# Performance work log

Measured on AMD Instinct MI355X. Metric: run time of the kernel, lower is better.

## Reference

```python
import jax, jax.numpy as jnp
import numpy as np

N_NODES = 50000
N_EDGES = 800000
IN_FEATS = 96
HIDDEN = 48


def setup_inputs() -> dict:
    key = jax.random.key(0)
    ks = jax.random.split(key, 16)
    x = jax.random.normal(ks[0], (N_NODES, IN_FEATS), dtype=jnp.float32)
    edge_index = jax.random.randint(ks[1], (2, N_EDGES), 0, N_NODES, dtype=jnp.int32)

    def lin(k, fan_in, fan_out):
        s = 1.0 / np.sqrt(fan_in)
        return jax.random.uniform(k, (fan_in, fan_out), jnp.float32, -s, s)

    return {
        "x": x,
        "edge_index": edge_index,
        # SAGEConv layer 0: in -> hidden
        "w_self0": lin(ks[2], IN_FEATS, HIDDEN),
        "w_neigh0": lin(ks[3], IN_FEATS, HIDDEN),
        "b0": jnp.zeros((HIDDEN,), jnp.float32),
        # SAGEConv layer 1: hidden -> hidden
        "w_self1": lin(ks[4], HIDDEN, HIDDEN),
        "w_neigh1": lin(ks[5], HIDDEN, HIDDEN),
        "b1": jnp.zeros((HIDDEN,), jnp.float32),
        # SAGEConv layer 2: hidden -> hidden
        "w_self2": lin(ks[6], HIDDEN, HIDDEN),
        "w_neigh2": lin(ks[7], HIDDEN, HIDDEN),
        "b2": jnp.zeros((HIDDEN,), jnp.float32),
        # prediction head: hidden -> 1
        "w_pred": lin(ks[8], HIDDEN, 1),
        "b_pred": jnp.zeros((1,), jnp.float32),
    }


def _sage_mean(x, src, dst, deg_inv, w_self, w_neigh, b):
    # mean over in-neighbors: gather src features, segment-sum at dst, / in-degree
    agg = jax.ops.segment_sum(x[src], dst, num_segments=N_NODES) * deg_inv  # [N, F]
    return x @ w_self + agg @ w_neigh + b


def reference(x, edge_index, w_self0, w_neigh0, b0, w_self1, w_neigh1, b1,
              w_self2, w_neigh2, b2, w_pred, b_pred):
    src, dst = edge_index[0], edge_index[1]
    deg = jax.ops.segment_sum(jnp.ones((src.shape[0],), x.dtype), dst,
                              num_segments=N_NODES)
    deg_inv = (1.0 / jnp.maximum(deg, 1.0))[:, None]  # isolated nodes -> 0 agg

    h = jax.nn.relu(_sage_mean(x, src, dst, deg_inv, w_self0, w_neigh0, b0))
    h = jax.nn.relu(_sage_mean(h, src, dst, deg_inv, w_self1, w_neigh1, b1))
    h = jax.nn.relu(_sage_mean(h, src, dst, deg_inv, w_self2, w_neigh2, b2))
    return h @ w_pred + b_pred  # [N, 1]
```

## Files before the change

### kernel.cpp

```cpp
#include <hip/hip_runtime.h>
#include <hip/hip_fp16.h>


constexpr int HID = 48;
constexpr int MAXDEG = 64;
constexpr int GNB = 64;

__device__ __forceinline__ unsigned pack_h2(float a, float b) {
    __half2 h = __floats2half2_rn(a, b);
    return *reinterpret_cast<unsigned*>(&h);
}
__device__ __forceinline__ void acc_u2(float* g, uint2 u) {
    __half2 h0 = *reinterpret_cast<__half2*>(&u.x);
    __half2 h1 = *reinterpret_cast<__half2*>(&u.y);
    float2 f0 = __half22float2(h0), f1 = __half22float2(h1);
    g[0] += f0.x; g[1] += f0.y; g[2] += f1.x; g[3] += f1.y;
}
__device__ __forceinline__ void unpack_u2(float* v, uint2 u) {
    __half2 h0 = *reinterpret_cast<__half2*>(&u.x);
    __half2 h1 = *reinterpret_cast<__half2*>(&u.y);
    float2 f0 = __half22float2(h0), f1 = __half22float2(h1);
    v[0] = f0.x; v[1] = f0.y; v[2] = f1.x; v[3] = f1.y;
}
__device__ __forceinline__ void fma12_h(const uint2* __restrict__ wrow, float s,
                                        float* acc) {
    uint2 w0 = wrow[0], w1 = wrow[1], w2 = wrow[2];
    float v[12];
    unpack_u2(v + 0, w0); unpack_u2(v + 4, w1); unpack_u2(v + 8, w2);
#pragma unroll
    for (int j = 0; j < 12; ++j) acc[j] = fmaf(s, v[j], acc[j]);
}

__device__ __forceinline__ void gather_h4(const __half* __restrict__ p,
                                          const unsigned short* __restrict__ bkt,
                                          int deg, int e, int jb, float* g) {
    float ga[12], gb[12];
#pragma unroll
    for (int j = 0; j < 12; ++j) { ga[j] = 0.0f; gb[j] = 0.0f; }
    int i = e;
    for (; i + 6 < deg; i += 8) {
        int s0 = bkt[i], s1 = bkt[i + 2], s2 = bkt[i + 4], s3 = bkt[i + 6];
        const uint2* r0 = reinterpret_cast<const uint2*>(p + (size_t)s0 * HID + jb);
        const uint2* r1 = reinterpret_cast<const uint2*>(p + (size_t)s1 * HID + jb);
        const uint2* r2 = reinterpret_cast<const uint2*>(p + (size_t)s2 * HID + jb);
        const uint2* r3 = reinterpret_cast<const uint2*>(p + (size_t)s3 * HID + jb);
        uint2 a0 = r0[0], a1 = r0[1], a2 = r0[2];
        uint2 b0 = r1[0], b1 = r1[1], b2 = r1[2];
        uint2 c0 = r2[0], c1 = r2[1], c2 = r2[2];
        uint2 d0 = r3[0], d1 = r3[1], d2 = r3[2];
        acc_u2(ga + 0, a0); acc_u2(ga + 4, a1); acc_u2(ga + 8, a2);
        acc_u2(gb + 0, b0); acc_u2(gb + 4, b1); acc_u2(gb + 8, b2);
        acc_u2(ga + 0, c0); acc_u2(ga + 4, c1); acc_u2(ga + 8, c2);
        acc_u2(gb + 0, d0); acc_u2(gb + 4, d1); acc_u2(gb + 8, d2);
    }
    for (; i + 2 < deg; i += 4) {
        int s0 = bkt[i], s1 = bkt[i + 2];
        const uint2* r0 = reinterpret_cast<const uint2*>(p + (size_t)s0 * HID + jb);
        const uint2* r1 = reinterpret_cast<const uint2*>(p + (size_t)s1 * HID + jb);
        uint2 a0 = r0[0], a1 = r0[1], a2 = r0[2];
        uint2 b0 = r1[0], b1 = r1[1], b2 = r1[2];
        acc_u2(ga + 0, a0); acc_u2(ga + 4, a1); acc_u2(ga + 8, a2);
        acc_u2(gb + 0, b0); acc_u2(gb + 4, b1); acc_u2(gb + 8, b2);
    }
    if (i < deg) {
        const uint2* r0 = reinterpret_cast<const uint2*>(p + (size_t)bkt[i] * HID + jb);
        uint2 a0 = r0[0], a1 = r0[1], a2 = r0[2];
        acc_u2(ga + 0, a0); acc_u2(ga + 4, a1); acc_u2(ga + 8, a2);
    }
#pragma unroll
    for (int j = 0; j < 12; ++j) g[j] = ga[j] + gb[j];
#pragma unroll
    for (int j = 0; j < 12; ++j) g[j] += __shfl_xor(g[j], 4, 64);
}

__global__ __launch_bounds__(128) void fill_proj_k(
    const float* __restrict__ X, const float* __restrict__ Wn,
    const float* __restrict__ Ws, const float* __restrict__ bias,
    __half* __restrict__ p_out, float* __restrict__ s_out, int n_nodes,
    const int* __restrict__ src, const int* __restrict__ dst,
    int* __restrict__ cnt, unsigned short* __restrict__ buckets,
    int n_edges, int gemm_blocks) {
    __shared__ float wlds[96 * HID];
    __shared__ float bias_lds[HID];
    const int t = threadIdx.x;

    if ((int)blockIdx.x >= gemm_blocks) {
        int base = (blockIdx.x - gemm_blocks) * 256 + t;
        int e0 = base, e1 = base + 128;
        if (e0 < n_edges) {
            int d = dst[e0];
            int s = src[e0];
            int pos = atomicAdd(&cnt[d], 1);
            if (pos < MAXDEG) buckets[(size_t)d * MAXDEG + pos] = (unsigned short)s;
        }
        if (e1 < n_edges) {
            int d = dst[e1];
            int s = src[e1];
            int pos = atomicAdd(&cnt[d], 1);
            if (pos < MAXDEG) buckets[(size_t)d * MAXDEG + pos] = (unsigned short)s;
        }
        return;
    }

    const int q = t & 3;
    const int m = t >> 2;
    const int jb = q * 12;
    const int n0 = blockIdx.x * GNB + 2 * m;
    const int n1 = n0 + 1;
    const bool v0 = n0 < n_nodes, v1 = n1 < n_nodes;
    const int cn0 = v0 ? n0 : 0, cn1 = v1 ? n1 : 0;
    const float4* xr0 = reinterpret_cast<const float4*>(X + (size_t)cn0 * 96);
    const float4* xr1 = reinterpret_cast<const float4*>(X + (size_t)cn1 * 96);

    for (int i = t; i < 96 * HID; i += 128) wlds[i] = Wn[i];
    __syncthreads();
    {
        float pa[12], pb[12];
#pragma unroll
        for (int j = 0; j < 12; ++j) { pa[j] = 0.0f; pb[j] = 0.0f; }
#pragma unroll 4
        for (int k4 = 0; k4 < 24; ++k4) {
            float4 xa = xr0[k4];
            float4 xb = xr1[k4];
#pragma unroll
            for (int c = 0; c < 4; ++c) {
                float x0 = (c == 0) ? xa.x : (c == 1) ? xa.y : (c == 2) ? xa.z : xa.w;
                float x1 = (c == 0) ? xb.x : (c == 1) ? xb.y : (c == 2) ? xb.z : xb.w;
                const float4* wr =
                    reinterpret_cast<const float4*>(&wlds[(k4 * 4 + c) * HID + jb]);
#pragma unroll
                for (int j4 = 0; j4 < 3; ++j4) {
                    float4 wv = wr[j4];
                    pa[j4 * 4 + 0] = fmaf(x0, wv.x, pa[j4 * 4 + 0]);
                    pa[j4 * 4 + 1] = fmaf(x0, wv.y, pa[j4 * 4 + 1]);
                    pa[j4 * 4 + 2] = fmaf(x0, wv.z, pa[j4 * 4 + 2]);
                    pa[j4 * 4 + 3] = fmaf(x0, wv.w, pa[j4 * 4 + 3]);
                    pb[j4 * 4 + 0] = fmaf(x1, wv.x, pb[j4 * 4 + 0]);
                    pb[j4 * 4 + 1] = fmaf(x1, wv.y, pb[j4 * 4 + 1]);
                    pb[j4 * 4 + 2] = fmaf(x1, wv.z, pb[j4 * 4 + 2]);
                    pb[j4 * 4 + 3] = fmaf(x1, wv.w, pb[j4 * 4 + 3]);
                }
            }
        }
        if (v0) {
            uint2* po = reinterpret_cast<uint2*>(p_out + (size_t)n0 * HID + jb);
            po[0] = make_uint2(pack_h2(pa[0], pa[1]), pack_h2(pa[2], pa[3]));
            po[1] = make_uint2(pack_h2(pa[4], pa[5]), pack_h2(pa[6], pa[7]));
            po[2] = make_uint2(pack_h2(pa[8], pa[9]), pack_h2(pa[10], pa[11]));
        }
        if (v1) {
            uint2* po = reinterpret_cast<uint2*>(p_out + (size_t)n1 * HID + jb);
            po[0] = make_uint2(pack_h2(pb[0], pb[1]), pack_h2(pb[2], pb[3]));
            po[1] = make_uint2(pack_h2(pb[4], pb[5]), pack_h2(pb[6], pb[7]));
            po[2] = make_uint2(pack_h2(pb[8], pb[9]), pack_h2(pb[10], pb[11]));
        }
    }
    __syncthreads();

    for (int i = t; i < 96 * HID; i += 128) wlds[i] = Ws[i];
    if (t < HID) bias_lds[t] = bias[t];
    __syncthreads();
    {
        float sa[12], sb[12];
#pragma unroll
        for (int j = 0; j < 12; ++j) {
            float b = bias_lds[jb + j];
            sa[j] = b; sb[j] = b;
        }
#pragma unroll 4
        for (int k4 = 0; k4 < 24; ++k4) {
            float4 xa = xr0[k4];
            float4 xb = xr1[k4];
#pragma unroll
            for (int c = 0; c < 4; ++c) {
                float x0 = (c == 0) ? xa.x : (c == 1) ? xa.y : (c == 2) ? xa.z : xa.w;
                float x1 = (c == 0) ? xb.x : (c == 1) ? xb.y : (c == 2) ? xb.z : xb.w;
                const float4* wr =
                    reinterpret_cast<const float4*>(&wlds[(k4 * 4 + c) * HID + jb]);
#pragma unroll
                for (int j4 = 0; j4 < 3; ++j4) {
                    float4 wv = wr[j4];
                    sa[j4 * 4 + 0] = fmaf(x0, wv.x, sa[j4 * 4 + 0]);
                    sa[j4 * 4 + 1] = fmaf(x0, wv.y, sa[j4 * 4 + 1]);
                    sa[j4 * 4 + 2] = fmaf(x0, wv.z, sa[j4 * 4 + 2]);
                    sa[j4 * 4 + 3] = fmaf(x0, wv.w, sa[j4 * 4 + 3]);
                    sb[j4 * 4 + 0] = fmaf(x1, wv.x, sb[j4 * 4 + 0]);
                    sb[j4 * 4 + 1] = fmaf(x1, wv.y, sb[j4 * 4 + 1]);
                    sb[j4 * 4 + 2] = fmaf(x1, wv.z, sb[j4 * 4 + 2]);
                    sb[j4 * 4 + 3] = fmaf(x1, wv.w, sb[j4 * 4 + 3]);
                }
            }
        }
        float4* so0 = reinterpret_cast<float4*>(s_out + (size_t)cn0 * HID + jb);
        float4* so1 = reinterpret_cast<float4*>(s_out + (size_t)cn1 * HID + jb);
#pragma unroll
        for (int j4 = 0; j4 < 3; ++j4) {
            if (v0) so0[j4] = make_float4(sa[j4 * 4 + 0], sa[j4 * 4 + 1],
                                          sa[j4 * 4 + 2], sa[j4 * 4 + 3]);
            if (v1) so1[j4] = make_float4(sb[j4 * 4 + 0], sb[j4 * 4 + 1],
                                          sb[j4 * 4 + 2], sb[j4 * 4 + 3]);
        }
    }
}

__global__ __launch_bounds__(128, 6) void act_k(
    const __half* __restrict__ p_in, const float* __restrict__ s_in,
    const int* __restrict__ cnt, const unsigned short* __restrict__ buckets,
    __half* __restrict__ h_out, int n_nodes) {
    const int t = threadIdx.x;
    const int q = t & 3;
    const int e = (t >> 2) & 1;
    const int m = t >> 3;
    const int n = blockIdx.x * 16 + m;
    if (n >= n_nodes) return;
    const int jb = q * 12;

    const int deg = min(cnt[n], MAXDEG);
    const float di = 1.0f / fmaxf((float)deg, 1.0f);
    float g[12];
    gather_h4(p_in, buckets + (size_t)n * MAXDEG, deg, e, jb, g);

    if (e == 0) {
        const float4* sr = reinterpret_cast<const float4*>(s_in + (size_t)n * HID + jb);
        float h[12];
#pragma unroll
        for (int j4 = 0; j4 < 3; ++j4) {
            float4 sv = sr[j4];
            h[j4 * 4 + 0] = fmaxf(fmaf(di, g[j4 * 4 + 0], sv.x), 0.0f);
            h[j4 * 4 + 1] = fmaxf(fmaf(di, g[j4 * 4 + 1], sv.y), 0.0f);
            h[j4 * 4 + 2] = fmaxf(fmaf(di, g[j4 * 4 + 2], sv.z), 0.0f);
            h[j4 * 4 + 3] = fmaxf(fmaf(di, g[j4 * 4 + 3], sv.w), 0.0f);
        }
        uint2* ho = reinterpret_cast<uint2*>(h_out + (size_t)n * HID + jb);
        ho[0] = make_uint2(pack_h2(h[0], h[1]), pack_h2(h[2], h[3]));
        ho[1] = make_uint2(pack_h2(h[4], h[5]), pack_h2(h[6], h[7]));
        ho[2] = make_uint2(pack_h2(h[8], h[9]), pack_h2(h[10], h[11]));
    }
}

template <bool LAST>
__global__ __launch_bounds__(128, 6) void layer_k(
    const __half* __restrict__ h_in, const int* __restrict__ cnt,
    const unsigned short* __restrict__ buckets, const float* __restrict__ wn,
    const float* __restrict__ ws, const float* __restrict__ bn,
    const float* __restrict__ w_pred, const float* __restrict__ b_pred,
    __half* __restrict__ h_out, float* __restrict__ out, int n_nodes) {
    __shared__ uint2 wn_s[HID * HID / 4];
    __shared__ uint2 ws_s[HID * HID / 4];
    __shared__ float bn_lds[HID];
    __shared__ float wp_lds[HID];

    const int t = threadIdx.x;
    for (int i4 = t; i4 < HID * HID / 4; i4 += 128) {
        float4 a = reinterpret_cast<const float4*>(wn)[i4];
        float4 b = reinterpret_cast<const float4*>(ws)[i4];
        wn_s[i4] = make_uint2(pack_h2(a.x, a.y), pack_h2(a.z, a.w));
        ws_s[i4] = make_uint2(pack_h2(b.x, b.y), pack_h2(b.z, b.w));
    }
    if (t < HID) bn_lds[t] = bn[t];
    if (LAST && t < HID) wp_lds[t] = w_pred[t];
    __syncthreads();

    const int q = t & 3;
    const int e = (t >> 2) & 1;
    const int m = t >> 3;
    const int n = blockIdx.x * 16 + m;
    if (n >= n_nodes) return;
    const int jb = q * 12;

    const int deg = min(cnt[n], MAXDEG);
    const float di = 1.0f / fmaxf((float)deg, 1.0f);
    float g[12];
    gather_h4(h_in, buckets + (size_t)n * MAXDEG, deg, e, jb, g);
#pragma unroll
    for (int j = 0; j < 12; ++j) g[j] *= di;

    float hs_own[12];
    {
        const uint2* hr = reinterpret_cast<const uint2*>(h_in + (size_t)n * HID + jb);
        uint2 a = hr[0], b = hr[1], c = hr[2];
        unpack_u2(hs_own + 0, a); unpack_u2(hs_own + 4, b); unpack_u2(hs_own + 8, c);
    }

    float acc[12];
#pragma unroll
    for (int j = 0; j < 12; ++j) acc[j] = (e == 0) ? bn_lds[jb + j] : 0.0f;

    const int kb = e * 24;
#pragma unroll
    for (int kk = 0; kk < 24; ++kk) {
        const int k = kb + kk;
        const int srcl = (t & ~3) | (k / 12);
        float gs = __shfl(g[kk % 12], srcl, 64);
        float hv = __shfl(hs_own[kk % 12], srcl, 64);
        fma12_h(&wn_s[(k * HID + jb) >> 2], gs, acc);
        fma12_h(&ws_s[(k * HID + jb) >> 2], hv, acc);
    }
#pragma unroll
    for (int j = 0; j < 12; ++j) acc[j] += __shfl_xor(acc[j], 4, 64);

    if (LAST) {
        float s = 0.0f;
#pragma unroll
        for (int j = 0; j < 12; ++j) s = fmaf(fmaxf(acc[j], 0.0f), wp_lds[jb + j], s);
        s += __shfl_xor(s, 1, 64);
        s += __shfl_xor(s, 2, 64);
        if ((t & 7) == 0) out[n] = s + b_pred[0];
        return;
    }

    if (e == 0) {
        float h[12];
#pragma unroll
        for (int j = 0; j < 12; ++j) h[j] = fmaxf(acc[j], 0.0f);
        uint2* ho = reinterpret_cast<uint2*>(h_out + (size_t)n * HID + jb);
        ho[0] = make_uint2(pack_h2(h[0], h[1]), pack_h2(h[2], h[3]));
        ho[1] = make_uint2(pack_h2(h[4], h[5]), pack_h2(h[6], h[7]));
        ho[2] = make_uint2(pack_h2(h[8], h[9]), pack_h2(h[10], h[11]));
    }
}

extern "C" void kernel_launch(void* const* d_in, const int* in_sizes, int n_in,
                              void* d_out, int out_size, void* d_ws, size_t ws_size,
                              hipStream_t stream) {
    const float* x        = (const float*)d_in[0];
    const int*   ei       = (const int*)d_in[1];
    const float* w_self0  = (const float*)d_in[2];
    const float* w_neigh0 = (const float*)d_in[3];
    const float* b0       = (const float*)d_in[4];
    const float* w_self1  = (const float*)d_in[5];
    const float* w_neigh1 = (const float*)d_in[6];
    const float* b1       = (const float*)d_in[7];
    const float* w_self2  = (const float*)d_in[8];
    const float* w_neigh2 = (const float*)d_in[9];
    const float* b2       = (const float*)d_in[10];
    const float* w_pred   = (const float*)d_in[11];
    const float* b_pred   = (const float*)d_in[12];

    const int n_nodes = in_sizes[0] / 96;
    const int n_edges = in_sizes[1] / 2;
    const int* src = ei;
    const int* dst = ei + n_edges;

    char* wsb = (char*)d_ws;
    int* cnt                = (int*)wsb;              wsb += (size_t)n_nodes * 4;
    unsigned short* buckets = (unsigned short*)wsb;   wsb += (size_t)n_nodes * MAXDEG * 2;
    __half* p0 = (__half*)wsb;                        wsb += (size_t)n_nodes * HID * 2;
    __half* h1 = (__half*)wsb;                        wsb += (size_t)n_nodes * HID * 2;
    __half* h2 = (__half*)wsb;                        wsb += (size_t)n_nodes * HID * 2;
    float* s0 = (float*)wsb;                          wsb += (size_t)n_nodes * HID * 4;
    float* out = (float*)d_out;

    const int gnb = (n_nodes + GNB - 1) / GNB;
    const int fb = (n_edges + 255) / 256;
    const int lb = (n_nodes + 15) / 16;

    hipMemsetAsync(cnt, 0, (size_t)n_nodes * 4, stream);

    fill_proj_k<<<gnb + fb, 128, 0, stream>>>(x, w_neigh0, w_self0, b0, p0, s0,
                                              n_nodes, src, dst, cnt, buckets,
                                              n_edges, gnb);
    act_k<<<lb, 128, 0, stream>>>(p0, s0, cnt, buckets, h1, n_nodes);
    layer_k<false><<<lb, 128, 0, stream>>>(h1, cnt, buckets, w_neigh1, w_self1,
                                           b1, nullptr, nullptr, h2, nullptr,
                                           n_nodes);
    layer_k<true><<<lb, 128, 0, stream>>>(h2, cnt, buckets, w_neigh2, w_self2,
                                          b2, w_pred, b_pred, nullptr, out,
                                          n_nodes);
}
```

Measured before the change: 208.7 us.

## Prefetch bucket indices and unroll first 16 neighbor gathers with zero-row padding

Loads the first 16 neighbor indices as two vector loads and gathers them unconditionally, substituting a zeroed padding row for slots beyond the degree, so more independent loads are in flight. Layer kernels issue the count, bucket and self-feature loads before the shared-memory weight fill so they overlap. Degree counters are spaced by a stride of 4 to reduce atomic contention, and the edge-fill blocks process 4 edges per thread. Low-degree nodes now issue extra loads of the padding row, and the workspace grows slightly.

```diff
diff --git a/kernel.cpp b/kernel.cpp
--- a/kernel.cpp
+++ b/kernel.cpp
@@ -31,13 +31,52 @@
     for (int j = 0; j < 12; ++j) acc[j] = fmaf(s, v[j], acc[j]);
 }
 
-__device__ __forceinline__ void gather_h4(const __half* __restrict__ p,
+__device__ __forceinline__ void gather_h8(const __half* __restrict__ p,
                                           const unsigned short* __restrict__ bkt,
-                                          int deg, int e, int jb, float* g) {
+                                          uint4 pv0, uint4 pv1, int deg, int e,
+                                          int jb, int zrow, float* g) {
     float ga[12], gb[12];
 #pragma unroll
     for (int j = 0; j < 12; ++j) { ga[j] = 0.0f; gb[j] = 0.0f; }
-    int i = e;
+    const int sh = 16 * e;
+    int idx[8];
+    {
+        unsigned w[8] = {pv0.x, pv0.y, pv0.z, pv0.w, pv1.x, pv1.y, pv1.z, pv1.w};
+#pragma unroll
+        for (int r = 0; r < 8; ++r) {
+            int k = 2 * r + e;
+            idx[r] = (k < deg) ? (int)((w[r] >> sh) & 0xffffu) : zrow;
+        }
+    }
+    {
+        const uint2* r0 = reinterpret_cast<const uint2*>(p + (size_t)idx[0] * HID + jb);
+        const uint2* r1 = reinterpret_cast<const uint2*>(p + (size_t)idx[1] * HID + jb);
+        const uint2* r2 = reinterpret_cast<const uint2*>(p + (size_t)idx[2] * HID + jb);
+        const uint2* r3 = reinterpret_cast<const uint2*>(p + (size_t)idx[3] * HID + jb);
+        uint2 a0 = r0[0], a1 = r0[1], a2 = r0[2];
+        uint2 b0 = r1[0], b1 = r1[1], b2 = r1[2];
+        uint2 c0 = r2[0], c1 = r2[1], c2 = r2[2];
+        uint2 d0 = r3[0], d1 = r3[1], d2 = r3[2];
+        acc_u2(ga + 0, a0); acc_u2(ga + 4, a1); acc_u2(ga + 8, a2);
+        acc_u2(gb + 0, b0); acc_u2(gb + 4, b1); acc_u2(gb + 8, b2);
+        acc_u2(ga + 0, c0); acc_u2(ga + 4, c1); acc_u2(ga + 8, c2);
+        acc_u2(gb + 0, d0); acc_u2(gb + 4, d1); acc_u2(gb + 8, d2);
+    }
+    {
+        const uint2* r0 = reinterpret_cast<const uint2*>(p + (size_t)idx[4] * HID + jb);
+        const uint2* r1 = reinterpret_cast<const uint2*>(p + (size_t)idx[5] * HID + jb);
+        const uint2* r2 = reinterpret_cast<const uint2*>(p + (size_t)idx[6] * HID + jb);
+        const uint2* r3 = reinterpret_cast<const uint2*>(p + (size_t)idx[7] * HID + jb);
+        uint2 a0 = r0[0], a1 = r0[1], a2 = r0[2];
+        uint2 b0 = r1[0], b1 = r1[1], b2 = r1[2];
+        uint2 c0 = r2[0], c1 = r2[1], c2 = r2[2];
+        uint2 d0 = r3[0], d1 = r3[1], d2 = r3[2];
+        acc_u2(ga + 0, a0); acc_u2(ga + 4, a1); acc_u2(ga + 8, a2);
+        acc_u2(gb + 0, b0); acc_u2(gb + 4, b1); acc_u2(gb + 8, b2);
+        acc_u2(ga + 0, c0); acc_u2(ga + 4, c1); acc_u2(ga + 8, c2);
+        acc_u2(gb + 0, d0); acc_u2(gb + 4, d1); acc_u2(gb + 8, d2);
+    }
+    int i = 16 + e;
     for (; i + 6 < deg; i += 8) {
         int s0 = bkt[i], s1 = bkt[i + 2], s2 = bkt[i + 4], s3 = bkt[i + 6];
         const uint2* r0 = reinterpret_cast<const uint2*>(p + (size_t)s0 * HID + jb);
@@ -79,28 +118,28 @@
     __half* __restrict__ p_out, float* __restrict__ s_out, int n_nodes,
     const int* __restrict__ src, const int* __restrict__ dst,
     int* __restrict__ cnt, unsigned short* __restrict__ buckets,
-    int n_edges, int gemm_blocks) {
+    int n_edges, int gemm_blocks, int cstride) {
     __shared__ float wlds[96 * HID];
     __shared__ float bias_lds[HID];
     const int t = threadIdx.x;
 
     if ((int)blockIdx.x >= gemm_blocks) {
-        int base = (blockIdx.x - gemm_blocks) * 256 + t;
-        int e0 = base, e1 = base + 128;
-        if (e0 < n_edges) {
-            int d = dst[e0];
-            int s = src[e0];
-            int pos = atomicAdd(&cnt[d], 1);
-            if (pos < MAXDEG) buckets[(size_t)d * MAXDEG + pos] = (unsigned short)s;
-        }
-        if (e1 < n_edges) {
-            int d = dst[e1];
-            int s = src[e1];
-            int pos = atomicAdd(&cnt[d], 1);
-            if (pos < MAXDEG) buckets[(size_t)d * MAXDEG + pos] = (unsigned short)s;
+        int base = (blockIdx.x - gemm_blocks) * 512 + t;
+#pragma unroll
+        for (int u = 0; u < 4; ++u) {
+            int eidx = base + u * 128;
+            if (eidx < n_edges) {
+                int d = dst[eidx];
+                int s = src[eidx];
+                int pos = atomicAdd(&cnt[(size_t)d * cstride], 1);
+                if (pos < MAXDEG) buckets[(size_t)d * MAXDEG + pos] = (unsigned short)s;
+            }
         }
         return;
     }
+
+    if (blockIdx.x == 0 && t < 24)
+        reinterpret_cast<unsigned*>(p_out + (size_t)n_nodes * HID)[t] = 0u;
 
     const int q = t & 3;
     const int m = t >> 2;
@@ -206,8 +245,10 @@
 __global__ __launch_bounds__(128, 6) void act_k(
     const __half* __restrict__ p_in, const float* __restrict__ s_in,
     const int* __restrict__ cnt, const unsigned short* __restrict__ buckets,
-    __half* __restrict__ h_out, int n_nodes) {
+    __half* __restrict__ h_out, int n_nodes, int cstride) {
     const int t = threadIdx.x;
+    if (blockIdx.x == 0 && t < 24)
+        reinterpret_cast<unsigned*>(h_out + (size_t)n_nodes * HID)[t] = 0u;
     const int q = t & 3;
     const int e = (t >> 2) & 1;
     const int m = t >> 3;
@@ -215,22 +256,35 @@
     if (n >= n_nodes) return;
     const int jb = q * 12;
 
-    const int deg = min(cnt[n], MAXDEG);
+    const int deg_raw = cnt[(size_t)n * cstride];
+    const unsigned short* bkt = buckets + (size_t)n * MAXDEG;
+    const uint4 pv0 = reinterpret_cast<const uint4*>(bkt)[0];
+    const uint4 pv1 = reinterpret_cast<const uint4*>(bkt)[1];
+    float4 sv0, sv1, sv2;
+    if (e == 0) {
+        const float4* sr = reinterpret_cast<const float4*>(s_in + (size_t)n * HID + jb);
+        sv0 = sr[0]; sv1 = sr[1]; sv2 = sr[2];
+    }
+
+    const int deg = min(deg_raw, MAXDEG);
     const float di = 1.0f / fmaxf((float)deg, 1.0f);
     float g[12];
-    gather_h4(p_in, buckets + (size_t)n * MAXDEG, deg, e, jb, g);
+    gather_h8(p_in, bkt, pv0, pv1, deg, e, jb, n_nodes, g);
 
     if (e == 0) {
-        const float4* sr = reinterpret_cast<const float4*>(s_in + (size_t)n * HID + jb);
         float h[12];
-#pragma unroll
-        for (int j4 = 0; j4 < 3; ++j4) {
-            float4 sv = sr[j4];
-            h[j4 * 4 + 0] = fmaxf(fmaf(di, g[j4 * 4 + 0], sv.x), 0.0f);
-            h[j4 * 4 + 1] = fmaxf(fmaf(di, g[j4 * 4 + 1], sv.y), 0.0f);
-            h[j4 * 4 + 2] = fmaxf(fmaf(di, g[j4 * 4 + 2], sv.z), 0.0f);
-            h[j4 * 4 + 3] = fmaxf(fmaf(di, g[j4 * 4 + 3], sv.w), 0.0f);
-        }
+        h[0] = fmaxf(fmaf(di, g[0], sv0.x), 0.0f);
+        h[1] = fmaxf(fmaf(di, g[1], sv0.y), 0.0f);
+        h[2] = fmaxf(fmaf(di, g[2], sv0.z), 0.0f);
+        h[3] = fmaxf(fmaf(di, g[3], sv0.w), 0.0f);
+        h[4] = fmaxf(fmaf(di, g[4], sv1.x), 0.0f);
+        h[5] = fmaxf(fmaf(di, g[5], sv1.y), 0.0f);
+        h[6] = fmaxf(fmaf(di, g[6], sv1.z), 0.0f);
+        h[7] = fmaxf(fmaf(di, g[7], sv1.w), 0.0f);
+        h[8] = fmaxf(fmaf(di, g[8], sv2.x), 0.0f);
+        h[9] = fmaxf(fmaf(di, g[9], sv2.y), 0.0f);
+        h[10] = fmaxf(fmaf(di, g[10], sv2.z), 0.0f);
+        h[11] = fmaxf(fmaf(di, g[11], sv2.w), 0.0f);
         uint2* ho = reinterpret_cast<uint2*>(h_out + (size_t)n * HID + jb);
         ho[0] = make_uint2(pack_h2(h[0], h[1]), pack_h2(h[2], h[3]));
         ho[1] = make_uint2(pack_h2(h[4], h[5]), pack_h2(h[6], h[7]));
@@ -244,13 +298,32 @@
     const unsigned short* __restrict__ buckets, const float* __restrict__ wn,
     const float* __restrict__ ws, const float* __restrict__ bn,
     const float* __restrict__ w_pred, const float* __restrict__ b_pred,
-    __half* __restrict__ h_out, float* __restrict__ out, int n_nodes) {
+    __half* __restrict__ h_out, float* __restrict__ out, int n_nodes,
+    int cstride) {
     __shared__ uint2 wn_s[HID * HID / 4];
     __shared__ uint2 ws_s[HID * HID / 4];
     __shared__ float bn_lds[HID];
     __shared__ float wp_lds[HID];
 
     const int t = threadIdx.x;
+    const int q = t & 3;
+    const int e = (t >> 2) & 1;
+    const int m = t >> 3;
+    const int n = blockIdx.x * 16 + m;
+    const bool nv = n < n_nodes;
+    const int cn = nv ? n : 0;
+    const int jb = q * 12;
+
+    if (!LAST && blockIdx.x == 0 && t < 24)
+        reinterpret_cast<unsigned*>(h_out + (size_t)n_nodes * HID)[t] = 0u;
+
+    const int deg_raw = cnt[(size_t)cn * cstride];
+    const unsigned short* bkt = buckets + (size_t)cn * MAXDEG;
+    const uint4 pv0 = reinterpret_cast<const uint4*>(bkt)[0];
+    const uint4 pv1 = reinterpret_cast<const uint4*>(bkt)[1];
+    const uint2* hr = reinterpret_cast<const uint2*>(h_in + (size_t)cn * HID + jb);
+    uint2 ha = hr[0], hb = hr[1], hc = hr[2];
+
     for (int i4 = t; i4 < HID * HID / 4; i4 += 128) {
         float4 a = reinterpret_cast<const float4*>(wn)[i4];
         float4 b = reinterpret_cast<const float4*>(ws)[i4];
@@ -261,26 +334,17 @@
     if (LAST && t < HID) wp_lds[t] = w_pred[t];
     __syncthreads();
 
-    const int q = t & 3;
-    const int e = (t >> 2) & 1;
-    const int m = t >> 3;
-    const int n = blockIdx.x * 16 + m;
-    if (n >= n_nodes) return;
-    const int jb = q * 12;
-
-    const int deg = min(cnt[n], MAXDEG);
+    if (!nv) return;
+
+    const int deg = min(deg_raw, MAXDEG);
     const float di = 1.0f / fmaxf((float)deg, 1.0f);
     float g[12];
-    gather_h4(h_in, buckets + (size_t)n * MAXDEG, deg, e, jb, g);
+    gather_h8(h_in, bkt, pv0, pv1, deg, e, jb, n_nodes, g);
 #pragma unroll
     for (int j = 0; j < 12; ++j) g[j] *= di;
 
     float hs_own[12];
-    {
-        const uint2* hr = reinterpret_cast<const uint2*>(h_in + (size_t)n * HID + jb);
-        uint2 a = hr[0], b = hr[1], c = hr[2];
-        unpack_u2(hs_own + 0, a); unpack_u2(hs_own + 4, b); unpack_u2(hs_own + 8, c);
-    }
+    unpack_u2(hs_own + 0, ha); unpack_u2(hs_own + 4, hb); unpack_u2(hs_own + 8, hc);
 
     float acc[12];
 #pragma unroll
@@ -342,29 +406,34 @@
     const int* src = ei;
     const int* dst = ei + n_edges;
 
+    const size_t need_fixed = (size_t)n_nodes * MAXDEG * 2
+                            + 3 * ((size_t)(n_nodes + 1) * HID * 2)
+                            + (size_t)n_nodes * HID * 4;
+    int cstride = (need_fixed + (size_t)n_nodes * 4 * 4 <= ws_size) ? 4 : 1;
+
     char* wsb = (char*)d_ws;
-    int* cnt                = (int*)wsb;              wsb += (size_t)n_nodes * 4;
+    int* cnt                = (int*)wsb;              wsb += (size_t)n_nodes * cstride * 4;
     unsigned short* buckets = (unsigned short*)wsb;   wsb += (size_t)n_nodes * MAXDEG * 2;
-    __half* p0 = (__half*)wsb;                        wsb += (size_t)n_nodes * HID * 2;
-    __half* h1 = (__half*)wsb;                        wsb += (size_t)n_nodes * HID * 2;
-    __half* h2 = (__half*)wsb;                        wsb += (size_t)n_nodes * HID * 2;
+    __half* p0 = (__half*)wsb;                        wsb += (size_t)(n_nodes + 1) * HID * 2;
+    __half* h1 = (__half*)wsb;                        wsb += (size_t)(n_nodes + 1) * HID * 2;
+    __half* h2 = (__half*)wsb;                        wsb += (size_t)(n_nodes + 1) * HID * 2;
     float* s0 = (float*)wsb;                          wsb += (size_t)n_nodes * HID * 4;
     float* out = (float*)d_out;
 
     const int gnb = (n_nodes + GNB - 1) / GNB;
-    const int fb = (n_edges + 255) / 256;
+    const int fb = (n_edges + 511) / 512;
     const int lb = (n_nodes + 15) / 16;
 
-    hipMemsetAsync(cnt, 0, (size_t)n_nodes * 4, stream);
+    hipMemsetAsync(cnt, 0, (size_t)n_nodes * cstride * 4, stream);
 
     fill_proj_k<<<gnb + fb, 128, 0, stream>>>(x, w_neigh0, w_self0, b0, p0, s0,
                                               n_nodes, src, dst, cnt, buckets,
-                                              n_edges, gnb);
-    act_k<<<lb, 128, 0, stream>>>(p0, s0, cnt, buckets, h1, n_nodes);
+                                              n_edges, gnb, cstride);
+    act_k<<<lb, 128, 0, stream>>>(p0, s0, cnt, buckets, h1, n_nodes, cstride);
     layer_k<false><<<lb, 128, 0, stream>>>(h1, cnt, buckets, w_neigh1, w_self1,
                                            b1, nullptr, nullptr, h2, nullptr,
-                                           n_nodes);
+                                           n_nodes, cstride);
     layer_k<true><<<lb, 128, 0, stream>>>(h2, cnt, buckets, w_neigh2, w_self2,
                                           b2, w_pred, b_pred, nullptr, out,
-                                          n_nodes);
-}
+                                          n_nodes, cstride);
+}
```

Result: slower. 216.6 us (+3.8%).

## Fuse all GNN stages into one persistent cooperative kernel with grid syncs

Applied to the files above, without the earlier changes.

Replaces the memset plus four kernel launches with a single cooperative persistent kernel. It zeroes the counts, runs projection and edge bucketing, activation, and two SAGE layers, separated by grid-wide syncs. Blocks loop over tiles of 32 nodes, and edge filling is split into 1024 larger chunks. The aim is to remove launch gaps and tail effects between stages, at the cost of grid-sync overhead, lower occupancy (launch bounds 4), and reduced parallelism per stage. A fallback path with multi-kernel launches is kept.

```diff
diff --git a/kernel.cpp b/kernel.cpp
--- a/kernel.cpp
+++ b/kernel.cpp
@@ -1,10 +1,15 @@
 #include <hip/hip_runtime.h>
 #include <hip/hip_fp16.h>
+#include <hip/hip_cooperative_groups.h>
+
+namespace cg = cooperative_groups;
 
 
 constexpr int HID = 48;
 constexpr int MAXDEG = 64;
 constexpr int GNB = 64;
+constexpr int NFILL = 1024;
+constexpr int TILE = 32;
 
 __device__ __forceinline__ unsigned pack_h2(float a, float b) {
     __half2 h = __floats2half2_rn(a, b);
@@ -73,39 +78,42 @@
     for (int j = 0; j < 12; ++j) g[j] += __shfl_xor(g[j], 4, 64);
 }
 
-__global__ __launch_bounds__(128) void fill_proj_k(
-    const float* __restrict__ X, const float* __restrict__ Wn,
-    const float* __restrict__ Ws, const float* __restrict__ bias,
-    __half* __restrict__ p_out, float* __restrict__ s_out, int n_nodes,
-    const int* __restrict__ src, const int* __restrict__ dst,
-    int* __restrict__ cnt, unsigned short* __restrict__ buckets,
-    int n_edges, int gemm_blocks) {
-    __shared__ float wlds[96 * HID];
-    __shared__ float bias_lds[HID];
-    const int t = threadIdx.x;
-
-    if ((int)blockIdx.x >= gemm_blocks) {
-        int base = (blockIdx.x - gemm_blocks) * 256 + t;
-        int e0 = base, e1 = base + 128;
-        if (e0 < n_edges) {
-            int d = dst[e0];
-            int s = src[e0];
-            int pos = atomicAdd(&cnt[d], 1);
-            if (pos < MAXDEG) buckets[(size_t)d * MAXDEG + pos] = (unsigned short)s;
-        }
-        if (e1 < n_edges) {
-            int d = dst[e1];
-            int s = src[e1];
-            int pos = atomicAdd(&cnt[d], 1);
-            if (pos < MAXDEG) buckets[(size_t)d * MAXDEG + pos] = (unsigned short)s;
-        }
-        return;
-    }
+__device__ __forceinline__ void dev_fill(int c, int ce, int n_edges,
+                                         const int* __restrict__ src,
+                                         const int* __restrict__ dst,
+                                         int* __restrict__ cnt,
+                                         unsigned short* __restrict__ buckets,
+                                         int t) {
+    const int e0 = c * ce;
+    const int e1 = min(e0 + ce, n_edges);
+    for (int i = e0 + t; i < e1; i += 512) {
+#pragma unroll
+        for (int u = 0; u < 4; ++u) {
+            int eidx = i + u * 128;
+            if (eidx < e1) {
+                int d = dst[eidx];
+                int s = src[eidx];
+                int pos = atomicAdd(&cnt[d], 1);
+                if (pos < MAXDEG) buckets[(size_t)d * MAXDEG + pos] = (unsigned short)s;
+            }
+        }
+    }
+}
+
+__device__ void dev_proj(int u, const float* __restrict__ X,
+                         const float* __restrict__ Wn,
+                         const float* __restrict__ Ws,
+                         const float* __restrict__ bias,
+                         __half* __restrict__ p_out,
+                         float* __restrict__ s_out, int n_nodes,
+                         float* __restrict__ smem, int t) {
+    float* wlds = smem;
+    float* bias_lds = smem + 96 * HID;
 
     const int q = t & 3;
     const int m = t >> 2;
     const int jb = q * 12;
-    const int n0 = blockIdx.x * GNB + 2 * m;
+    const int n0 = u * GNB + 2 * m;
     const int n1 = n0 + 1;
     const bool v0 = n0 < n_nodes, v1 = n1 < n_nodes;
     const int cn0 = v0 ? n0 : 0, cn1 = v1 ? n1 : 0;
@@ -203,15 +211,16 @@
     }
 }
 
-__global__ __launch_bounds__(128, 6) void act_k(
-    const __half* __restrict__ p_in, const float* __restrict__ s_in,
-    const int* __restrict__ cnt, const unsigned short* __restrict__ buckets,
-    __half* __restrict__ h_out, int n_nodes) {
-    const int t = threadIdx.x;
+__device__ __forceinline__ void dev_act16(int base, const __half* __restrict__ p_in,
+                                          const float* __restrict__ s_in,
+                                          const int* __restrict__ cnt,
+                                          const unsigned short* __restrict__ buckets,
+                                          __half* __restrict__ h_out, int n_nodes,
+                                          int t) {
     const int q = t & 3;
     const int e = (t >> 2) & 1;
     const int m = t >> 3;
-    const int n = blockIdx.x * 16 + m;
+    const int n = base + m;
     if (n >= n_nodes) return;
     const int jb = q * 12;
 
@@ -222,15 +231,20 @@
 
     if (e == 0) {
         const float4* sr = reinterpret_cast<const float4*>(s_in + (size_t)n * HID + jb);
+        float4 sv0 = sr[0], sv1 = sr[1], sv2 = sr[2];
         float h[12];
-#pragma unroll
-        for (int j4 = 0; j4 < 3; ++j4) {
-            float4 sv = sr[j4];
-            h[j4 * 4 + 0] = fmaxf(fmaf(di, g[j4 * 4 + 0], sv.x), 0.0f);
-            h[j4 * 4 + 1] = fmaxf(fmaf(di, g[j4 * 4 + 1], sv.y), 0.0f);
-            h[j4 * 4 + 2] = fmaxf(fmaf(di, g[j4 * 4 + 2], sv.z), 0.0f);
-            h[j4 * 4 + 3] = fmaxf(fmaf(di, g[j4 * 4 + 3], sv.w), 0.0f);
-        }
+        h[0] = fmaxf(fmaf(di, g[0], sv0.x), 0.0f);
+        h[1] = fmaxf(fmaf(di, g[1], sv0.y), 0.0f);
+        h[2] = fmaxf(fmaf(di, g[2], sv0.z), 0.0f);
+        h[3] = fmaxf(fmaf(di, g[3], sv0.w), 0.0f);
+        h[4] = fmaxf(fmaf(di, g[4], sv1.x), 0.0f);
+        h[5] = fmaxf(fmaf(di, g[5], sv1.y), 0.0f);
+        h[6] = fmaxf(fmaf(di, g[6], sv1.z), 0.0f);
+        h[7] = fmaxf(fmaf(di, g[7], sv1.w), 0.0f);
+        h[8] = fmaxf(fmaf(di, g[8], sv2.x), 0.0f);
+        h[9] = fmaxf(fmaf(di, g[9], sv2.y), 0.0f);
+        h[10] = fmaxf(fmaf(di, g[10], sv2.z), 0.0f);
+        h[11] = fmaxf(fmaf(di, g[11], sv2.w), 0.0f);
         uint2* ho = reinterpret_cast<uint2*>(h_out + (size_t)n * HID + jb);
         ho[0] = make_uint2(pack_h2(h[0], h[1]), pack_h2(h[2], h[3]));
         ho[1] = make_uint2(pack_h2(h[4], h[5]), pack_h2(h[6], h[7]));
@@ -238,33 +252,41 @@
     }
 }
 
-template <bool LAST>
-__global__ __launch_bounds__(128, 6) void layer_k(
-    const __half* __restrict__ h_in, const int* __restrict__ cnt,
-    const unsigned short* __restrict__ buckets, const float* __restrict__ wn,
-    const float* __restrict__ ws, const float* __restrict__ bn,
-    const float* __restrict__ w_pred, const float* __restrict__ b_pred,
-    __half* __restrict__ h_out, float* __restrict__ out, int n_nodes) {
-    __shared__ uint2 wn_s[HID * HID / 4];
-    __shared__ uint2 ws_s[HID * HID / 4];
-    __shared__ float bn_lds[HID];
-    __shared__ float wp_lds[HID];
-
-    const int t = threadIdx.x;
+__device__ __forceinline__ void stage_layer(const float* __restrict__ wn,
+                                            const float* __restrict__ ws,
+                                            const float* __restrict__ bn,
+                                            const float* __restrict__ wp,
+                                            bool last, float* __restrict__ smem,
+                                            int t) {
+    uint2* wn_s = reinterpret_cast<uint2*>(smem);
+    uint2* ws_s = reinterpret_cast<uint2*>(smem + 1152);
     for (int i4 = t; i4 < HID * HID / 4; i4 += 128) {
         float4 a = reinterpret_cast<const float4*>(wn)[i4];
         float4 b = reinterpret_cast<const float4*>(ws)[i4];
         wn_s[i4] = make_uint2(pack_h2(a.x, a.y), pack_h2(a.z, a.w));
         ws_s[i4] = make_uint2(pack_h2(b.x, b.y), pack_h2(b.z, b.w));
     }
-    if (t < HID) bn_lds[t] = bn[t];
-    if (LAST && t < HID) wp_lds[t] = w_pred[t];
-    __syncthreads();
+    if (t < HID) smem[2304 + t] = bn[t];
+    if (last && t < HID) smem[2352 + t] = wp[t];
+}
+
+template <bool LAST>
+__device__ __forceinline__ void dev_layer16(int base, const __half* __restrict__ h_in,
+                                            const int* __restrict__ cnt,
+                                            const unsigned short* __restrict__ buckets,
+                                            const float* __restrict__ b_pred,
+                                            __half* __restrict__ h_out,
+                                            float* __restrict__ out, int n_nodes,
+                                            float* __restrict__ smem, int t) {
+    uint2* wn_s = reinterpret_cast<uint2*>(smem);
+    uint2* ws_s = reinterpret_cast<uint2*>(smem + 1152);
+    float* bn_lds = smem + 2304;
+    float* wp_lds = smem + 2352;
 
     const int q = t & 3;
     const int e = (t >> 2) & 1;
     const int m = t >> 3;
-    const int n = blockIdx.x * 16 + m;
+    const int n = base + m;
     if (n >= n_nodes) return;
     const int jb = q * 12;
 
@@ -318,6 +340,104 @@
         ho[1] = make_uint2(pack_h2(h[4], h[5]), pack_h2(h[6], h[7]));
         ho[2] = make_uint2(pack_h2(h[8], h[9]), pack_h2(h[10], h[11]));
     }
+}
+
+__global__ __launch_bounds__(128, 4) void persist_k(
+    const float* __restrict__ X, const int* __restrict__ src,
+    const int* __restrict__ dst,
+    const float* __restrict__ wn0, const float* __restrict__ ws0,
+    const float* __restrict__ b0,
+    const float* __restrict__ wn1, const float* __restrict__ ws1,
+    const float* __restrict__ b1,
+    const float* __restrict__ wn2, const float* __restrict__ ws2,
+    const float* __restrict__ b2,
+    const float* __restrict__ w_pred, const float* __restrict__ b_pred,
+    int* __restrict__ cnt, unsigned short* __restrict__ buckets,
+    __half* __restrict__ p0, __half* __restrict__ h1, __half* __restrict__ h2,
+    float* __restrict__ s0, float* __restrict__ out,
+    int n_nodes, int n_edges, int nproj, int ce, int ntile) {
+    __shared__ __align__(16) float smem[96 * HID + 64];
+    cg::grid_group grid = cg::this_grid();
+    const int bid = blockIdx.x;
+    const int G = gridDim.x;
+    const int t = threadIdx.x;
+
+    for (int i = bid * 128 + t; i < n_nodes; i += G * 128) cnt[i] = 0;
+    grid.sync();
+
+    for (int u = bid; u < nproj + NFILL; u += G) {
+        if (u < nproj)
+            dev_proj(u, X, wn0, ws0, b0, p0, s0, n_nodes, smem, t);
+        else
+            dev_fill(u - nproj, ce, n_edges, src, dst, cnt, buckets, t);
+    }
+    grid.sync();
+
+    for (int u = bid; u < ntile; u += G) {
+        dev_act16(u * TILE, p0, s0, cnt, buckets, h1, n_nodes, t);
+        dev_act16(u * TILE + 16, p0, s0, cnt, buckets, h1, n_nodes, t);
+    }
+    grid.sync();
+
+    stage_layer(wn1, ws1, b1, nullptr, false, smem, t);
+    __syncthreads();
+    for (int u = bid; u < ntile; u += G) {
+        dev_layer16<false>(u * TILE, h1, cnt, buckets, nullptr, h2, nullptr,
+                           n_nodes, smem, t);
+        dev_layer16<false>(u * TILE + 16, h1, cnt, buckets, nullptr, h2, nullptr,
+                           n_nodes, smem, t);
+    }
+    grid.sync();
+
+    stage_layer(wn2, ws2, b2, w_pred, true, smem, t);
+    __syncthreads();
+    for (int u = bid; u < ntile; u += G) {
+        dev_layer16<true>(u * TILE, h2, cnt, buckets, b_pred, nullptr, out,
+                          n_nodes, smem, t);
+        dev_layer16<true>(u * TILE + 16, h2, cnt, buckets, b_pred, nullptr, out,
+                          n_nodes, smem, t);
+    }
+}
+
+__global__ __launch_bounds__(128) void fb_fill_proj_k(
+    const float* __restrict__ X, const float* __restrict__ Wn,
+    const float* __restrict__ Ws, const float* __restrict__ bias,
+    __half* __restrict__ p_out, float* __restrict__ s_out, int n_nodes,
+    const int* __restrict__ src, const int* __restrict__ dst,
+    int* __restrict__ cnt, unsigned short* __restrict__ buckets,
+    int n_edges, int nproj, int ce) {
+    __shared__ __align__(16) float smem[96 * HID + 64];
+    const int t = threadIdx.x;
+    if ((int)blockIdx.x < nproj)
+        dev_proj(blockIdx.x, X, Wn, Ws, bias, p_out, s_out, n_nodes, smem, t);
+    else
+        dev_fill(blockIdx.x - nproj, ce, n_edges, src, dst, cnt, buckets, t);
+}
+
+__global__ __launch_bounds__(128, 6) void fb_act_k(
+    const __half* __restrict__ p_in, const float* __restrict__ s_in,
+    const int* __restrict__ cnt, const unsigned short* __restrict__ buckets,
+    __half* __restrict__ h_out, int n_nodes) {
+    const int t = threadIdx.x;
+    dev_act16(blockIdx.x * TILE, p_in, s_in, cnt, buckets, h_out, n_nodes, t);
+    dev_act16(blockIdx.x * TILE + 16, p_in, s_in, cnt, buckets, h_out, n_nodes, t);
+}
+
+template <bool LAST>
+__global__ __launch_bounds__(128, 6) void fb_layer_k(
+    const __half* __restrict__ h_in, const int* __restrict__ cnt,
+    const unsigned short* __restrict__ buckets, const float* __restrict__ wn,
+    const float* __restrict__ ws, const float* __restrict__ bn,
+    const float* __restrict__ w_pred, const float* __restrict__ b_pred,
+    __half* __restrict__ h_out, float* __restrict__ out, int n_nodes) {
+    __shared__ __align__(16) float smem[2432];
+    const int t = threadIdx.x;
+    stage_layer(wn, ws, bn, w_pred, LAST, smem, t);
+    __syncthreads();
+    dev_layer16<LAST>(blockIdx.x * TILE, h_in, cnt, buckets, b_pred, h_out, out,
+                      n_nodes, smem, t);
+    dev_layer16<LAST>(blockIdx.x * TILE + 16, h_in, cnt, buckets, b_pred, h_out,
+                      out, n_nodes, smem, t);
 }
 
 extern "C" void kernel_launch(void* const* d_in, const int* in_sizes, int n_in,
@@ -351,20 +471,55 @@
     float* s0 = (float*)wsb;                          wsb += (size_t)n_nodes * HID * 4;
     float* out = (float*)d_out;
 
-    const int gnb = (n_nodes + GNB - 1) / GNB;
-    const int fb = (n_edges + 255) / 256;
-    const int lb = (n_nodes + 15) / 16;
+    int nproj = (n_nodes + GNB - 1) / GNB;
+    int ce    = (n_edges + NFILL - 1) / NFILL;
+    int ntile = (n_nodes + TILE - 1) / TILE;
+
+    static int coop_grid = -2;
+    if (coop_grid == -2) {
+        int dev = 0;
+        hipGetDevice(&dev);
+        int coop = 0;
+        hipDeviceGetAttribute(&coop, hipDeviceAttributeCooperativeLaunch, dev);
+        hipDeviceProp_t prop;
+        hipGetDeviceProperties(&prop, dev);
+        int nb = 0;
+        hipOccupancyMaxActiveBlocksPerMultiprocessor(&nb, persist_k, 128, 0);
+        if (coop && nb > 0) {
+            long g = (long)nb * prop.multiProcessorCount;
+            if (g > 2048) g = 2048;
+            coop_grid = (int)g;
+        } else {
+            coop_grid = -1;
+        }
+    }
+
+    if (coop_grid > 0) {
+        void* kp[] = {
+            (void*)&x, (void*)&src, (void*)&dst,
+            (void*)&w_neigh0, (void*)&w_self0, (void*)&b0,
+            (void*)&w_neigh1, (void*)&w_self1, (void*)&b1,
+            (void*)&w_neigh2, (void*)&w_self2, (void*)&b2,
+            (void*)&w_pred, (void*)&b_pred,
+            (void*)&cnt, (void*)&buckets,
+            (void*)&p0, (void*)&h1, (void*)&h2, (void*)&s0, (void*)&out,
+            (void*)&n_nodes, (void*)&n_edges, (void*)&nproj, (void*)&ce,
+            (void*)&ntile};
+        hipError_t err = hipLaunchCooperativeKernel(
+            (const void*)persist_k, dim3(coop_grid), dim3(128), kp, 0, stream);
+        if (err == hipSuccess) return;
+        coop_grid = -1;
+    }
 
     hipMemsetAsync(cnt, 0, (size_t)n_nodes * 4, stream);
-
-    fill_proj_k<<<gnb + fb, 128, 0, stream>>>(x, w_neigh0, w_self0, b0, p0, s0,
-                                              n_nodes, src, dst, cnt, buckets,
-                                              n_edges, gnb);
-    act_k<<<lb, 128, 0, stream>>>(p0, s0, cnt, buckets, h1, n_nodes);
-    layer_k<false><<<lb, 128, 0, stream>>>(h1, cnt, buckets, w_neigh1, w_self1,
-                                           b1, nullptr, nullptr, h2, nullptr,
-                                           n_nodes);
-    layer_k<true><<<lb, 128, 0, stream>>>(h2, cnt, buckets, w_neigh2, w_self2,
-                                          b2, w_pred, b_pred, nullptr, out,
-                                          n_nodes);
-}
+    fb_fill_proj_k<<<nproj + NFILL, 128, 0, stream>>>(
+        x, w_neigh0, w_self0, b0, p0, s0, n_nodes, src, dst, cnt, buckets,
+        n_edges, nproj, ce);
+    fb_act_k<<<ntile, 128, 0, stream>>>(p0, s0, cnt, buckets, h1, n_nodes);
+    fb_layer_k<false><<<ntile, 128, 0, stream>>>(h1, cnt, buckets, w_neigh1,
+                                                 w_self1, b1, nullptr, nullptr,
+                                                 h2, nullptr, n_nodes);
+    fb_layer_k<true><<<ntile, 128, 0, stream>>>(h2, cnt, buckets, w_neigh2,
+                                                w_self2, b2, w_pred, b_pred,
+                                                nullptr, out, n_nodes);
+}
```

Result: slower. 675.5 us (+223.7%).
